# Optimization experiments

Hardware: AMD Instinct MI355X
Metric: run time of the kernel (lower is better)

## Reference

```python
import jax, jax.numpy as jnp
import numpy as np
import math

H = 768          # bert hidden size
N_HYPO = 384     # number of hyponym instance embeddings
N_HYPER = 384    # number of hypernym instance embeddings
NUM_LABELS = 3


def setup_inputs() -> dict:
    key = jax.random.key(0)
    k1, k2, k3 = jax.random.split(key, 3)
    return {
        "hypo_embeddings": jax.random.normal(k1, (N_HYPO, H), dtype=jnp.float32),
        "hyper_embeddings": jax.random.normal(k2, (N_HYPER, H), dtype=jnp.float32),
        "W_cls": jax.random.normal(k3, (NUM_LABELS, 4 * H), dtype=jnp.float32) * 0.02,
        "b_cls": jnp.zeros((NUM_LABELS,), dtype=jnp.float32),
    }


def reference(hypo_embeddings, hyper_embeddings, W_cls, b_cls):
    h = hypo_embeddings.shape[-1]
    inv_sqrt_h = 1.0 / math.sqrt(h)
    # elementwise outer-product attention score: tanh(x_i * y_j) summed over hidden
    # [n_hypo, n_hyper, h] intermediate -> [n_hypo, n_hyper]
    att = jnp.tanh(hypo_embeddings[:, None, :] * hyper_embeddings[None, :, :]).sum(-1) * inv_sqrt_h

    hypo_side_att = jax.nn.softmax(att, axis=-1)   # rows attend over hypers
    hyper_side_att = jax.nn.softmax(att, axis=0)   # cols attend over hypos

    hyper_typ = hypo_side_att.sum(axis=0)
    hyper_typ = hyper_typ / hyper_typ.sum()
    hypo_typ = hyper_side_att.sum(axis=-1)
    hypo_typ = hypo_typ / hypo_typ.sum()

    # typicalness-weighted prototype pooling
    hyper_prototype = jnp.einsum('nm,md,n->d', hypo_side_att, hyper_embeddings, hypo_typ)
    hypo_prototype = jnp.einsum('nm,nd,m->d', hyper_side_att, hypo_embeddings, hyper_typ)

    feats = jnp.concatenate([
        hyper_prototype,
        hypo_prototype,
        hyper_prototype - hypo_prototype,
        hyper_prototype * hypo_prototype,
    ])  # [4h]
    sub_pred = W_cls @ feats + b_cls  # [num_labels]
    return sub_pred
```

## Files before the change

kernel.cpp:

```cpp
#include <hip/hip_runtime.h>

#define NN 384
#define HH 768
#define HP 772
#define L2E 1.4426950408889634f
#define TWO_L2E 2.8853900817779268f
#define INV_SQRT_H 0.03608439182435161f
#define ATT_L2E (INV_SQRT_H * L2E)
#define TCLAMP 25.0f

__device__ __forceinline__ float exp2_hw(float x) { return __builtin_amdgcn_exp2f(x); }
__device__ __forceinline__ float rcp_hw(float x) { return __builtin_amdgcn_rcpf(x); }

#define WS_E(ws)      ((ws))
#define WS_ET(ws)     ((ws) + NN * NN)
#define WS_ROWP(ws)   ((ws) + 2 * NN * NN)
#define WS_COLP(ws)   ((ws) + 2 * NN * NN + 48 * NN)
#define WS_ROWRS(ws)  ((ws) + 2 * NN * NN + 96 * NN)
#define WS_COLRS(ws)  (WS_ROWRS(ws) + NN)
#define WS_HYPERT(ws) (WS_COLRS(ws) + NN)
#define WS_HYPOT(ws)  (WS_HYPERT(ws) + NN)
#define WS_HP(ws)     (WS_HYPOT(ws) + NN)
#define WS_HQ(ws)     (WS_HP(ws) + HH)

__global__ __launch_bounds__(256) void k_att(const float* __restrict__ X,
                                             const float* __restrict__ Y,
                                             float* __restrict__ ws) {
    __shared__ float smem[16 * HP + 256];
    float* xs = smem;
    float* ys = smem + 8 * HP;
    float* part = smem + 16 * HP;
    float* E = WS_E(ws);
    float* ET = WS_ET(ws);
    float* rowP = WS_ROWP(ws);
    float* colP = WS_COLP(ws);

    const int tid = threadIdx.x;
    const int tt = blockIdx.x;
    const int it = tt / 48, jt = tt - it * 48;
    const int i0 = it * 8, j0 = jt * 8;

    const float4* gx = (const float4*)(X + i0 * HH);
    const float4* gy = (const float4*)(Y + j0 * HH);
#pragma unroll
    for (int p = 0; p < 6; p++) {
        int e = tid + p * 256;
        int r = e / 192, c = e - r * 192;
        float4 vx = gx[e];
        float4 vy = gy[e];
        ((float4*)(xs + r * HP))[c] = vx;
        vy.x *= TWO_L2E; vy.y *= TWO_L2E; vy.z *= TWO_L2E; vy.w *= TWO_L2E;
        ((float4*)(ys + r * HP))[c] = vy;
    }
    __syncthreads();

    const int wv = tid >> 6, ln = tid & 63;
    const int i = ln >> 3, j = ln & 7;
    const float4* xr = (const float4*)(xs + i * HP) + wv * 48;
    const float4* yr = (const float4*)(ys + j * HP) + wv * 48;
    float s = 0.f;
#pragma unroll 8
    for (int m = 0; m < 48; m++) {
        float4 a4 = xr[m];
        float4 b4 = yr[m];
        float t0 = fminf(a4.x * b4.x, TCLAMP);
        float t1 = fminf(a4.y * b4.y, TCLAMP);
        float t2 = fminf(a4.z * b4.z, TCLAMP);
        float t3 = fminf(a4.w * b4.w, TCLAMP);
        float pa = exp2_hw(t0) + 1.f;
        float pb = exp2_hw(t1) + 1.f;
        float pc = exp2_hw(t2) + 1.f;
        float pd = exp2_hw(t3) + 1.f;
        float ab = pa * pb, cd = pc * pd;
        float num = (pa + pb) * cd + (pc + pd) * ab;
        s = fmaf(num, rcp_hw(ab * cd), s);
    }
    part[wv * 64 + ln] = s;
    __syncthreads();
    if (tid < 64) {
        float t = part[tid] + part[64 + tid] + part[128 + tid] + part[192 + tid];
        float ev = exp2_hw((768.f - 2.f * t) * ATT_L2E);
        int ii = tid >> 3, jj = tid & 7;
        E[(i0 + ii) * NN + (j0 + jj)] = ev;
        ET[(j0 + jj) * NN + (i0 + ii)] = ev;
        float rs = ev;
        rs += __shfl_xor(rs, 1, 64); rs += __shfl_xor(rs, 2, 64); rs += __shfl_xor(rs, 4, 64);
        if (jj == 0) rowP[jt * NN + i0 + ii] = rs;
        float cs = ev;
        cs += __shfl_xor(cs, 8, 64); cs += __shfl_xor(cs, 16, 64); cs += __shfl_xor(cs, 32, 64);
        if (ii == 0) colP[it * NN + j0 + jj] = cs;
    }
}

__global__ __launch_bounds__(256) void k_typ(float* __restrict__ ws) {
    __shared__ float red[4];
    const int b = blockIdx.x, tid = threadIdx.x;
    const float* E = WS_E(ws);
    const float* ET = WS_ET(ws);
    const bool isCol = b < NN;
    const int x = isCol ? b : b - NN;
    const float* P = isCol ? WS_ROWP(ws) : WS_COLP(ws);
    const float* M = isCol ? ET : E;

    if (b == 1) {
        float* pz = WS_HP(ws);
#pragma unroll
        for (int q = 0; q < 6; q++) pz[tid + q * 256] = 0.f;
    }

    float s1 = 0.f, s2 = 0.f;
#pragma unroll 8
    for (int k = 0; k < 48; k++) {
        s1 += P[k * NN + tid];
        if (tid < 128) s2 += P[k * NN + tid + 256];
    }
    float r1 = rcp_hw(s1);
    float acc = M[x * NN + tid] * r1;
    float r2 = 0.f;
    if (tid < 128) {
        r2 = rcp_hw(s2);
        acc += M[x * NN + tid + 256] * r2;
    }
    if (isCol ? (b == 0) : (b == NN)) {
        float* RS = isCol ? WS_ROWRS(ws) : WS_COLRS(ws);
        RS[tid] = r1;
        if (tid < 128) RS[tid + 256] = r2;
    }
#pragma unroll
    for (int o = 32; o; o >>= 1) acc += __shfl_xor(acc, o, 64);
    if ((tid & 63) == 0) red[tid >> 6] = acc;
    __syncthreads();
    if (tid == 0) {
        float S = (red[0] + red[1]) + (red[2] + red[3]);
        (isCol ? WS_HYPERT(ws) : WS_HYPOT(ws))[x] = S * (1.f / NN);
    }
}

__global__ __launch_bounds__(256) void k_wp(const float* __restrict__ X,
                                            const float* __restrict__ Y,
                                            float* __restrict__ ws) {
    __shared__ float red[4];
    const int bb = blockIdx.x, tid = threadIdx.x;
    const bool hyperSide = bb < 48;
    const int jbase = (hyperSide ? bb : bb - 48) * 8;
    const float* M  = hyperSide ? WS_ET(ws) : WS_E(ws);
    const float* RS = hyperSide ? WS_ROWRS(ws) : WS_COLRS(ws);
    const float* T  = hyperSide ? WS_HYPOT(ws) : WS_HYPERT(ws);
    const float* V  = hyperSide ? Y : X;
    float* proto    = hyperSide ? WS_HP(ws) : WS_HQ(ws);

    float p0 = 0.f, p1 = 0.f, p2 = 0.f;
#pragma unroll
    for (int q = 0; q < 8; q++) {
        const int jj = jbase + q;
        float acc = M[jj * NN + tid] * RS[tid] * T[tid];
        if (tid < 128) acc += M[jj * NN + tid + 256] * RS[tid + 256] * T[tid + 256];
#pragma unroll
        for (int o = 32; o; o >>= 1) acc += __shfl_xor(acc, o, 64);
        if ((tid & 63) == 0) red[tid >> 6] = acc;
        __syncthreads();
        const float wj = (red[0] + red[1]) + (red[2] + red[3]);
        p0 = fmaf(wj, V[jj * HH + tid], p0);
        p1 = fmaf(wj, V[jj * HH + tid + 256], p1);
        p2 = fmaf(wj, V[jj * HH + tid + 512], p2);
        __syncthreads();
    }
    atomicAdd(proto + tid, p0);
    atomicAdd(proto + tid + 256, p1);
    atomicAdd(proto + tid + 512, p2);
}

__global__ __launch_bounds__(256) void k_cls(const float* __restrict__ W,
                                             const float* __restrict__ bias,
                                             const float* __restrict__ ws,
                                             float* __restrict__ out) {
    __shared__ float red[3][4];
    const int t = threadIdx.x;
    const float* hp = WS_HP((float*)ws);
    const float* hq = WS_HQ((float*)ws);
    float acc0 = 0.f, acc1 = 0.f, acc2 = 0.f;
    for (int d = t; d < 4 * HH; d += 256) {
        int seg = d / HH, r = d - seg * HH;
        float f = (seg == 0) ? hp[r] : (seg == 1) ? hq[r] : (seg == 2) ? (hp[r] - hq[r]) : (hp[r] * hq[r]);
        acc0 += W[d] * f;
        acc1 += W[3072 + d] * f;
        acc2 += W[6144 + d] * f;
    }
#pragma unroll
    for (int o = 32; o; o >>= 1) {
        acc0 += __shfl_xor(acc0, o, 64);
        acc1 += __shfl_xor(acc1, o, 64);
        acc2 += __shfl_xor(acc2, o, 64);
    }
    if ((t & 63) == 0) {
        red[0][t >> 6] = acc0;
        red[1][t >> 6] = acc1;
        red[2][t >> 6] = acc2;
    }
    __syncthreads();
    if (t < 3)
        out[t] = red[t][0] + red[t][1] + red[t][2] + red[t][3] + bias[t];
}

extern "C" void kernel_launch(void* const* d_in, const int* in_sizes, int n_in,
                              void* d_out, int out_size, void* d_ws, size_t ws_size,
                              hipStream_t stream) {
    const float* X = (const float*)d_in[0];
    const float* Y = (const float*)d_in[1];
    const float* W = (const float*)d_in[2];
    const float* B = (const float*)d_in[3];
    float* out = (float*)d_out;
    float* ws = (float*)d_ws;

    k_att<<<2304, 256, 0, stream>>>(X, Y, ws);
    k_typ<<<768, 256, 0, stream>>>(ws);
    k_wp<<<96, 256, 0, stream>>>(X, Y, ws);
    k_cls<<<1, 256, 0, stream>>>(W, B, ws, out);
}
```

Measured before the change: 116.3 us.

## Use 16x16 register-blocked attention tiles with per-element sigmoid form

The attention kernel moves from 8x8 tiles to 16x16 tiles. Each thread now computes a 2x2 block, so every shared-memory load is reused across four products. The hidden dimension is staged in two chunks to keep shared memory small. The tanh sum switches from a four-way batched reciprocal to one exp2 plus one reciprocal per element, which drops the clamp but issues four times as many transcendental reciprocals. Partial row and column sums shrink to 24 tiles, and the prototype-buffer zeroing moves from the typicality kernel into the attention kernel.

```diff
diff --git a/kernel.cpp b/kernel.cpp
--- a/kernel.cpp
+++ b/kernel.cpp
@@ -2,12 +2,12 @@
 
 #define NN 384
 #define HH 768
-#define HP 772
+#define RP 388
 #define L2E 1.4426950408889634f
 #define TWO_L2E 2.8853900817779268f
 #define INV_SQRT_H 0.03608439182435161f
 #define ATT_L2E (INV_SQRT_H * L2E)
-#define TCLAMP 25.0f
+#define NT 24
 
 __device__ __forceinline__ float exp2_hw(float x) { return __builtin_amdgcn_exp2f(x); }
 __device__ __forceinline__ float rcp_hw(float x) { return __builtin_amdgcn_rcpf(x); }
@@ -15,8 +15,8 @@
 #define WS_E(ws)      ((ws))
 #define WS_ET(ws)     ((ws) + NN * NN)
 #define WS_ROWP(ws)   ((ws) + 2 * NN * NN)
-#define WS_COLP(ws)   ((ws) + 2 * NN * NN + 48 * NN)
-#define WS_ROWRS(ws)  ((ws) + 2 * NN * NN + 96 * NN)
+#define WS_COLP(ws)   (WS_ROWP(ws) + NT * NN)
+#define WS_ROWRS(ws)  (WS_COLP(ws) + NT * NN)
 #define WS_COLRS(ws)  (WS_ROWRS(ws) + NN)
 #define WS_HYPERT(ws) (WS_COLRS(ws) + NN)
 #define WS_HYPOT(ws)  (WS_HYPERT(ws) + NN)
@@ -26,69 +26,98 @@
 __global__ __launch_bounds__(256) void k_att(const float* __restrict__ X,
                                              const float* __restrict__ Y,
                                              float* __restrict__ ws) {
-    __shared__ float smem[16 * HP + 256];
-    float* xs = smem;
-    float* ys = smem + 8 * HP;
-    float* part = smem + 16 * HP;
+    __shared__ float smem[32 * RP];
     float* E = WS_E(ws);
     float* ET = WS_ET(ws);
     float* rowP = WS_ROWP(ws);
     float* colP = WS_COLP(ws);
 
     const int tid = threadIdx.x;
-    const int tt = blockIdx.x;
-    const int it = tt / 48, jt = tt - it * 48;
-    const int i0 = it * 8, j0 = jt * 8;
-
-    const float4* gx = (const float4*)(X + i0 * HH);
-    const float4* gy = (const float4*)(Y + j0 * HH);
-#pragma unroll
-    for (int p = 0; p < 6; p++) {
-        int e = tid + p * 256;
-        int r = e / 192, c = e - r * 192;
-        float4 vx = gx[e];
-        float4 vy = gy[e];
-        ((float4*)(xs + r * HP))[c] = vx;
-        vy.x *= TWO_L2E; vy.y *= TWO_L2E; vy.z *= TWO_L2E; vy.w *= TWO_L2E;
-        ((float4*)(ys + r * HP))[c] = vy;
-    }
-    __syncthreads();
+    const int bb = blockIdx.x;
+    const int bi = bb / NT, bj = bb - bi * NT;
+    const int i0 = bi * 16, j0 = bj * 16;
+
+    if (bb == 0) {
+        float* pz = WS_HP(ws);
+#pragma unroll
+        for (int q = 0; q < 6; q++) pz[tid + q * 256] = 0.f;
+    }
 
     const int wv = tid >> 6, ln = tid & 63;
-    const int i = ln >> 3, j = ln & 7;
-    const float4* xr = (const float4*)(xs + i * HP) + wv * 48;
-    const float4* yr = (const float4*)(ys + j * HP) + wv * 48;
-    float s = 0.f;
-#pragma unroll 8
-    for (int m = 0; m < 48; m++) {
-        float4 a4 = xr[m];
-        float4 b4 = yr[m];
-        float t0 = fminf(a4.x * b4.x, TCLAMP);
-        float t1 = fminf(a4.y * b4.y, TCLAMP);
-        float t2 = fminf(a4.z * b4.z, TCLAMP);
-        float t3 = fminf(a4.w * b4.w, TCLAMP);
-        float pa = exp2_hw(t0) + 1.f;
-        float pb = exp2_hw(t1) + 1.f;
-        float pc = exp2_hw(t2) + 1.f;
-        float pd = exp2_hw(t3) + 1.f;
-        float ab = pa * pb, cd = pc * pd;
-        float num = (pa + pb) * cd + (pc + pd) * ab;
-        s = fmaf(num, rcp_hw(ab * cd), s);
-    }
-    part[wv * 64 + ln] = s;
-    __syncthreads();
-    if (tid < 64) {
-        float t = part[tid] + part[64 + tid] + part[128 + tid] + part[192 + tid];
-        float ev = exp2_hw((768.f - 2.f * t) * ATT_L2E);
-        int ii = tid >> 3, jj = tid & 7;
-        E[(i0 + ii) * NN + (j0 + jj)] = ev;
-        ET[(j0 + jj) * NN + (i0 + ii)] = ev;
-        float rs = ev;
-        rs += __shfl_xor(rs, 1, 64); rs += __shfl_xor(rs, 2, 64); rs += __shfl_xor(rs, 4, 64);
-        if (jj == 0) rowP[jt * NN + i0 + ii] = rs;
-        float cs = ev;
-        cs += __shfl_xor(cs, 8, 64); cs += __shfl_xor(cs, 16, 64); cs += __shfl_xor(cs, 32, 64);
-        if (ii == 0) colP[it * NN + j0 + jj] = cs;
+    const int r = ln >> 3, c = ln & 7;
+    float a00 = 0.f, a01 = 0.f, a10 = 0.f, a11 = 0.f;
+
+#pragma unroll
+    for (int ch = 0; ch < 2; ch++) {
+        const int kbase = ch * 384;
+#pragma unroll
+        for (int p = 0; p < 12; p++) {
+            int e = tid + p * 256;
+            int row = e / 96, col = e - row * 96;
+            float4 v;
+            if (row < 16) {
+                v = *(const float4*)(X + (i0 + row) * HH + kbase + col * 4);
+            } else {
+                v = *(const float4*)(Y + (j0 + row - 16) * HH + kbase + col * 4);
+                v.x *= TWO_L2E; v.y *= TWO_L2E; v.z *= TWO_L2E; v.w *= TWO_L2E;
+            }
+            *(float4*)(smem + row * RP + col * 4) = v;
+        }
+        __syncthreads();
+
+        const float4* xa = (const float4*)(smem + r * RP) + wv * 24;
+        const float4* xb = (const float4*)(smem + (r + 8) * RP) + wv * 24;
+        const float4* ya = (const float4*)(smem + (16 + c) * RP) + wv * 24;
+        const float4* yb = (const float4*)(smem + (24 + c) * RP) + wv * 24;
+#pragma unroll 6
+        for (int m = 0; m < 24; m++) {
+            float4 x0 = xa[m], x1 = xb[m], y0 = ya[m], y1 = yb[m];
+            a00 += rcp_hw(exp2_hw(x0.x * y0.x) + 1.f);
+            a00 += rcp_hw(exp2_hw(x0.y * y0.y) + 1.f);
+            a00 += rcp_hw(exp2_hw(x0.z * y0.z) + 1.f);
+            a00 += rcp_hw(exp2_hw(x0.w * y0.w) + 1.f);
+            a01 += rcp_hw(exp2_hw(x0.x * y1.x) + 1.f);
+            a01 += rcp_hw(exp2_hw(x0.y * y1.y) + 1.f);
+            a01 += rcp_hw(exp2_hw(x0.z * y1.z) + 1.f);
+            a01 += rcp_hw(exp2_hw(x0.w * y1.w) + 1.f);
+            a10 += rcp_hw(exp2_hw(x1.x * y0.x) + 1.f);
+            a10 += rcp_hw(exp2_hw(x1.y * y0.y) + 1.f);
+            a10 += rcp_hw(exp2_hw(x1.z * y0.z) + 1.f);
+            a10 += rcp_hw(exp2_hw(x1.w * y0.w) + 1.f);
+            a11 += rcp_hw(exp2_hw(x1.x * y1.x) + 1.f);
+            a11 += rcp_hw(exp2_hw(x1.y * y1.y) + 1.f);
+            a11 += rcp_hw(exp2_hw(x1.z * y1.z) + 1.f);
+            a11 += rcp_hw(exp2_hw(x1.w * y1.w) + 1.f);
+        }
+        __syncthreads();
+    }
+
+    float* part = smem;
+    part[wv * 256 + r * 16 + c]            = a00;
+    part[wv * 256 + r * 16 + c + 8]        = a01;
+    part[wv * 256 + (r + 8) * 16 + c]      = a10;
+    part[wv * 256 + (r + 8) * 16 + c + 8]  = a11;
+    __syncthreads();
+
+    float s = part[tid] + part[256 + tid] + part[512 + tid] + part[768 + tid];
+    float ev = exp2_hw((768.f - 2.f * s) * ATT_L2E);
+    const int rr = tid >> 4, cc = tid & 15;
+    E[(i0 + rr) * NN + (j0 + cc)] = ev;
+    ET[(j0 + cc) * NN + (i0 + rr)] = ev;
+
+    float rs = ev;
+    rs += __shfl_xor(rs, 1, 64); rs += __shfl_xor(rs, 2, 64);
+    rs += __shfl_xor(rs, 4, 64); rs += __shfl_xor(rs, 8, 64);
+    if (cc == 0) rowP[bj * NN + i0 + rr] = rs;
+
+    __syncthreads();
+    part[tid] = ev;
+    __syncthreads();
+    if (tid < 16) {
+        float cs = 0.f;
+#pragma unroll
+        for (int q = 0; q < 16; q++) cs += part[q * 16 + tid];
+        colP[bi * NN + j0 + tid] = cs;
     }
 }
 
@@ -102,15 +131,9 @@
     const float* P = isCol ? WS_ROWP(ws) : WS_COLP(ws);
     const float* M = isCol ? ET : E;
 
-    if (b == 1) {
-        float* pz = WS_HP(ws);
-#pragma unroll
-        for (int q = 0; q < 6; q++) pz[tid + q * 256] = 0.f;
-    }
-
     float s1 = 0.f, s2 = 0.f;
 #pragma unroll 8
-    for (int k = 0; k < 48; k++) {
+    for (int k = 0; k < NT; k++) {
         s1 += P[k * NN + tid];
         if (tid < 128) s2 += P[k * NN + tid + 256];
     }
@@ -212,7 +235,7 @@
     float* out = (float*)d_out;
     float* ws = (float*)d_ws;
 
-    k_att<<<2304, 256, 0, stream>>>(X, Y, ws);
+    k_att<<<576, 256, 0, stream>>>(X, Y, ws);
     k_typ<<<768, 256, 0, stream>>>(ws);
     k_wp<<<96, 256, 0, stream>>>(X, Y, ws);
     k_cls<<<1, 256, 0, stream>>>(W, B, ws, out);
```

Result: no change. 118.1 us (+1.6%).

## Stage attention tiles in hidden-dim chunks and use per-element sigmoid rcp

Applied to the files above, without the earlier changes.

The attention kernel now loads X and Y tiles in three 256-wide chunks into a much smaller shared buffer, which lets more blocks sit on each CU (the launch-bounds hint asks for 6). The inner loop drops the clamp and the batched four-way reciprocal in favour of one rcp per element, giving more transcendental ops but a shorter dependency chain and fewer registers. Zeroing of the prototype accumulators moves from the typicalness kernel into the attention kernel. The chunked scheme adds two extra barriers per chunk, and removing the clamp can let exp2 overflow to inf, though rcp(inf) returns 0 so the result stays valid.

```diff
diff --git a/kernel.cpp b/kernel.cpp
--- a/kernel.cpp
+++ b/kernel.cpp
@@ -2,12 +2,12 @@
 
 #define NN 384
 #define HH 768
-#define HP 772
+#define CHUNK 256
+#define CROW 260
 #define L2E 1.4426950408889634f
 #define TWO_L2E 2.8853900817779268f
 #define INV_SQRT_H 0.03608439182435161f
 #define ATT_L2E (INV_SQRT_H * L2E)
-#define TCLAMP 25.0f
 
 __device__ __forceinline__ float exp2_hw(float x) { return __builtin_amdgcn_exp2f(x); }
 __device__ __forceinline__ float rcp_hw(float x) { return __builtin_amdgcn_rcpf(x); }
@@ -23,13 +23,11 @@
 #define WS_HP(ws)     (WS_HYPOT(ws) + NN)
 #define WS_HQ(ws)     (WS_HP(ws) + HH)
 
-__global__ __launch_bounds__(256) void k_att(const float* __restrict__ X,
-                                             const float* __restrict__ Y,
-                                             float* __restrict__ ws) {
-    __shared__ float smem[16 * HP + 256];
-    float* xs = smem;
-    float* ys = smem + 8 * HP;
-    float* part = smem + 16 * HP;
+__global__ __launch_bounds__(256, 6) void k_att(const float* __restrict__ X,
+                                                const float* __restrict__ Y,
+                                                float* __restrict__ ws) {
+    __shared__ float smem[16 * CROW];
+    __shared__ float part[4][64];
     float* E = WS_E(ws);
     float* ET = WS_ET(ws);
     float* rowP = WS_ROWP(ws);
@@ -40,46 +38,52 @@
     const int it = tt / 48, jt = tt - it * 48;
     const int i0 = it * 8, j0 = jt * 8;
 
-    const float4* gx = (const float4*)(X + i0 * HH);
-    const float4* gy = (const float4*)(Y + j0 * HH);
-#pragma unroll
-    for (int p = 0; p < 6; p++) {
-        int e = tid + p * 256;
-        int r = e / 192, c = e - r * 192;
-        float4 vx = gx[e];
-        float4 vy = gy[e];
-        ((float4*)(xs + r * HP))[c] = vx;
-        vy.x *= TWO_L2E; vy.y *= TWO_L2E; vy.z *= TWO_L2E; vy.w *= TWO_L2E;
-        ((float4*)(ys + r * HP))[c] = vy;
-    }
-    __syncthreads();
+    if (tt == 0) {
+        float* pz = WS_HP(ws);
+#pragma unroll
+        for (int q = 0; q < 6; q++) pz[tid + q * 256] = 0.f;
+    }
 
     const int wv = tid >> 6, ln = tid & 63;
     const int i = ln >> 3, j = ln & 7;
-    const float4* xr = (const float4*)(xs + i * HP) + wv * 48;
-    const float4* yr = (const float4*)(ys + j * HP) + wv * 48;
-    float s = 0.f;
-#pragma unroll 8
-    for (int m = 0; m < 48; m++) {
-        float4 a4 = xr[m];
-        float4 b4 = yr[m];
-        float t0 = fminf(a4.x * b4.x, TCLAMP);
-        float t1 = fminf(a4.y * b4.y, TCLAMP);
-        float t2 = fminf(a4.z * b4.z, TCLAMP);
-        float t3 = fminf(a4.w * b4.w, TCLAMP);
-        float pa = exp2_hw(t0) + 1.f;
-        float pb = exp2_hw(t1) + 1.f;
-        float pc = exp2_hw(t2) + 1.f;
-        float pd = exp2_hw(t3) + 1.f;
-        float ab = pa * pb, cd = pc * pd;
-        float num = (pa + pb) * cd + (pc + pd) * ab;
-        s = fmaf(num, rcp_hw(ab * cd), s);
-    }
-    part[wv * 64 + ln] = s;
+    float a0 = 0.f, a1 = 0.f, a2 = 0.f, a3 = 0.f;
+
+#pragma unroll
+    for (int ch = 0; ch < 3; ch++) {
+#pragma unroll
+        for (int p = 0; p < 4; p++) {
+            int e = tid + p * 256;
+            int row = e >> 6, col = e & 63;
+            float4 v;
+            if (row < 8) {
+                v = *(const float4*)(X + (i0 + row) * HH + ch * CHUNK + col * 4);
+            } else {
+                v = *(const float4*)(Y + (j0 + row - 8) * HH + ch * CHUNK + col * 4);
+                v.x *= TWO_L2E; v.y *= TWO_L2E; v.z *= TWO_L2E; v.w *= TWO_L2E;
+            }
+            *(float4*)(smem + row * CROW + col * 4) = v;
+        }
+        __syncthreads();
+
+        const float4* xr = (const float4*)(smem + i * CROW) + wv * 16;
+        const float4* yr = (const float4*)(smem + (8 + j) * CROW) + wv * 16;
+#pragma unroll
+        for (int m = 0; m < 16; m++) {
+            float4 a = xr[m];
+            float4 b = yr[m];
+            a0 += rcp_hw(exp2_hw(a.x * b.x) + 1.f);
+            a1 += rcp_hw(exp2_hw(a.y * b.y) + 1.f);
+            a2 += rcp_hw(exp2_hw(a.z * b.z) + 1.f);
+            a3 += rcp_hw(exp2_hw(a.w * b.w) + 1.f);
+        }
+        __syncthreads();
+    }
+
+    part[wv][ln] = (a0 + a1) + (a2 + a3);
     __syncthreads();
     if (tid < 64) {
-        float t = part[tid] + part[64 + tid] + part[128 + tid] + part[192 + tid];
-        float ev = exp2_hw((768.f - 2.f * t) * ATT_L2E);
+        float s = part[0][tid] + part[1][tid] + part[2][tid] + part[3][tid];
+        float ev = exp2_hw((768.f - 2.f * s) * ATT_L2E);
         int ii = tid >> 3, jj = tid & 7;
         E[(i0 + ii) * NN + (j0 + jj)] = ev;
         ET[(j0 + jj) * NN + (i0 + ii)] = ev;
@@ -101,12 +105,6 @@
     const int x = isCol ? b : b - NN;
     const float* P = isCol ? WS_ROWP(ws) : WS_COLP(ws);
     const float* M = isCol ? ET : E;
-
-    if (b == 1) {
-        float* pz = WS_HP(ws);
-#pragma unroll
-        for (int q = 0; q < 6; q++) pz[tid + q * 256] = 0.f;
-    }
 
     float s1 = 0.f, s2 = 0.f;
 #pragma unroll 8
```

Result: slower. 447.2 us (+284.6%).
